# Kernel optimization log

Measured on AMD Instinct MI355X. Metric: run time of the kernel, lower is better.

Reference implementation:

```python
import jax, jax.numpy as jnp
import numpy as np

N = 262144   # number of units (batched instances of the module)
G = 128      # universe_field side length
D = 128      # dimension
RADIUS = 3   # min(3, G//2) == 3

# First D=128 neighborhood offsets in the original triple-loop order (i-major, j, k)
_grid = np.stack(np.meshgrid(np.arange(-RADIUS, RADIUS + 1),
                             np.arange(-RADIUS, RADIUS + 1),
                             np.arange(-RADIUS, RADIUS + 1), indexing='ij'), -1).reshape(-1, 3)[:D]
OI = jnp.asarray(_grid[:, 0], dtype=jnp.int32)
OJ = jnp.asarray(_grid[:, 1], dtype=jnp.int32)
OK = jnp.asarray(_grid[:, 2], dtype=jnp.int32)


def setup_inputs() -> dict:
    key = jax.random.key(0)
    ks = jax.random.split(key, 8)
    return {
        'universe_field': jax.random.normal(ks[0], (G, G, G), jnp.float32),
        'positions': jax.random.uniform(ks[1], (N, 3), jnp.float32) * G,
        'signatures': jax.random.normal(ks[2], (N, D), jnp.float32),
        'offsets': jax.random.normal(ks[3], (N, 3), jnp.float32) * 0.1,
        'W1': jax.random.normal(ks[4], (2 * D, D), jnp.float32) * (1.0 / np.sqrt(2 * D)),
        'b1': jax.random.normal(ks[5], (D,), jnp.float32) * 0.01,
        'W2': jax.random.normal(ks[6], (D, D), jnp.float32) * (1.0 / np.sqrt(D)),
        'b2': jax.random.normal(ks[7], (D,), jnp.float32) * 0.01,
    }


def _sample_local(field, pos):
    # pos: [N,3] float; truncate to int (torch .long()) then clamp, like the original
    pc = jnp.clip(jax.lax.stop_gradient(pos).astype(jnp.int32), 0, G - 1)  # [N,3]
    xx = jnp.clip(pc[:, 0:1] + OI[None, :], 0, G - 1)  # [N,D]
    yy = jnp.clip(pc[:, 1:2] + OJ[None, :], 0, G - 1)
    zz = jnp.clip(pc[:, 2:3] + OK[None, :], 0, G - 1)
    return field[xx, yy, zz]  # [N,D] gathered local field (343 points truncated to D)


def _stability(field, pos, signatures, W1, b1, W2, b2):
    local = _sample_local(field, pos)                       # [N,D]
    combined = jnp.concatenate([signatures, local], axis=-1)  # [N,2D]
    h = jnp.tanh(combined @ W1 + b1)                        # [N,D]
    resp = h @ W2 + b2                                      # [N,D]
    return jnp.linalg.norm(resp - signatures, axis=-1)      # [N]


def reference(universe_field, positions, signatures, offsets, W1, b1, W2, b2):
    stab_old = _stability(universe_field, positions, signatures, W1, b1, W2, b2)
    test_pos = positions + offsets
    stab_new = _stability(universe_field, test_pos, signatures, W1, b1, W2, b2)
    accept = stab_new <= stab_old                           # revert move if new_stab > old_stab
    final_pos = jnp.where(accept[:, None], test_pos, positions)
    stability = jnp.where(accept, stab_new, stab_old)
    return stability, final_pos
```

## Files before the change

### kernel.cpp

```cpp
#include <hip/hip_runtime.h>
#include <hip/hip_bf16.h>

#define NU 262144
#define GG 128
#define PG 134
#define DD 128

typedef __attribute__((ext_vector_type(8))) short short8;
typedef __attribute__((ext_vector_type(4))) float f32x4;

union Frag { short8 s; unsigned u[4]; };

__device__ __forceinline__ unsigned short f2b(float f) {
  union { float f; unsigned u; } v; v.f = f;
  unsigned r = v.u + 0x7fffu + ((v.u >> 16) & 1u);
  return (unsigned short)(r >> 16);
}
__device__ __forceinline__ unsigned cvtpk(float lo, float hi) {
  unsigned r;
  asm("v_cvt_pk_bf16_f32 %0, %1, %2" : "=v"(r) : "v"(lo), "v"(hi));
  return r;
}
__device__ __forceinline__ float unplo(unsigned w) {
  union { unsigned u; float f; } v; v.u = w << 16; return v.f;
}
__device__ __forceinline__ float unphi(unsigned w) {
  union { unsigned u; float f; } v; v.u = w & 0xffff0000u; return v.f;
}

__device__ __forceinline__ float fast_tanh(float x) {
  float e = __expf(fabsf(x) * 2.0f);
  float r = __frcp_rn(e + 1.0f);
  return copysignf(fmaf(-2.0f, r, 1.0f), x);
}

struct alignas(16) RowdT { int v[20]; };
static constexpr RowdT mkrowd() {
  RowdT t{};
  for (int r = 0; r < 20; ++r) {
    int rr = (r < 18) ? r : 18;
    int di = (rr < 18) ? (-3 + rr / 7) : -1;
    int dj = (rr < 18) ? (-3 + rr % 7) : 1;
    t.v[r] = (di * PG + dj) * PG - 3;
  }
  return t;
}
__device__ constexpr RowdT ROWD = mkrowd();

__global__ void prep_field(const float* __restrict__ f, unsigned short* __restrict__ fp) {
  int idx = blockIdx.x * 256 + threadIdx.x;
  if (idx >= PG * PG * PG) return;
  int z = idx % PG, t = idx / PG;
  int y = t % PG, x = t / PG;
  int xx = min(max(x - 3, 0), GG - 1);
  int yy = min(max(y - 3, 0), GG - 1);
  int zz = min(max(z - 3, 0), GG - 1);
  fp[idx] = f2b(f[(xx * GG + yy) * GG + zz]);
}

__global__ void prep_w(const float* __restrict__ W1, const float* __restrict__ W2,
                       unsigned short* __restrict__ wall) {
  int idx = blockIdx.x * 256 + threadIdx.x;
  if (idx >= 6656) return;
  int kt = idx >> 9, nt = (idx >> 6) & 7, ln = idx & 63;
  int n = nt * 16 + (ln & 15), lg = ln >> 4;
  short8 s;
  if (kt < 4) {
    int k0 = kt * 32 + lg * 8;
#pragma unroll
    for (int j = 0; j < 8; ++j) s[j] = (short)f2b(W1[(k0 + j) * DD + n]);
  } else if (kt < 9) {
    int r = (kt - 4) * 4 + lg;
#pragma unroll
    for (int j = 0; j < 8; ++j) {
      bool valid = (r < 18 && j < 7) || (r == 18 && j < 2);
      int row = 128 + ((r < 18) ? (r * 7 + j) : (126 + j));
      s[j] = valid ? (short)f2b(W1[row * DD + n]) : (short)0;
    }
  } else {
    int k0 = (kt - 9) * 32 + lg * 8;
#pragma unroll
    for (int j = 0; j < 8; ++j) s[j] = (short)f2b(W2[(k0 + j) * DD + n]);
  }
  ((short8*)wall)[idx] = s;
}

__global__ __launch_bounds__(512, 4) void atu_main(
    const float* __restrict__ pos, const float* __restrict__ sig,
    const float* __restrict__ offs,
    const float* __restrict__ b1, const float* __restrict__ b2,
    const unsigned short* __restrict__ fpad, const unsigned short* __restrict__ wall,
    float* __restrict__ out_stab, float* __restrict__ out_pos)
{
  __shared__ unsigned short ldsw[2][8192];
  __shared__ unsigned short lds12[4096];
  __shared__ alignas(16) unsigned short ns[8][2048];
  const int tid  = threadIdx.x;
  const int lane = tid & 63;
  const int lg   = lane >> 4, lm = lane & 15;
  const int wid  = tid >> 6;
  int bid = blockIdx.x;
  int swz = (bid & 7) * 256 + (bid >> 3);
  const int ub = swz * 128 + wid * 16;
  const int un = ub + lm;
  char* nsb = (char*)&ns[wid][0];
  const char* wallb = (const char*)wall;
  const char* fpadb = (const char*)fpad;

  int abase[2];
  {
    float px = pos[un * 3 + 0], py = pos[un * 3 + 1], pz = pos[un * 3 + 2];
    float qx = px + offs[un * 3 + 0], qy = py + offs[un * 3 + 1], qz = pz + offs[un * 3 + 2];
    int ax = min(max((int)px, 0), GG - 1), ay = min(max((int)py, 0), GG - 1), az = min(max((int)pz, 0), GG - 1);
    int bx = min(max((int)qx, 0), GG - 1), by = min(max((int)qy, 0), GG - 1), bz = min(max((int)qz, 0), GG - 1);
    abase[0] = ((ax + 3) * PG + (ay + 3)) * PG + (az + 3);
    abase[1] = ((bx + 3) * PG + (by + 3)) * PG + (bz + 3);
  }

#define GLL2(KTA, H)                                                              \
  __builtin_amdgcn_global_load_lds(                                               \
      (const unsigned*)(wallb + (((KTA) * 512 + tid) * 16)),                      \
      (unsigned*)((char*)&ldsw[H][0] + wid * 1024), 16, 0, 0);                    \
  __builtin_amdgcn_global_load_lds(                                               \
      (const unsigned*)(wallb + ((((KTA) + 1) * 512 + tid) * 16)),                \
      (unsigned*)((char*)&ldsw[H][0] + 8192 + wid * 1024), 16, 0, 0);

  GLL2(0, 0)
  __builtin_amdgcn_global_load_lds(
      (const unsigned*)(wallb + ((12 * 512 + tid) * 16)),
      (unsigned*)((char*)lds12 + wid * 1024), 16, 0, 0);
  f32x4 spa = *(const f32x4*)(sig + (size_t)un * DD + lg * 8);
  f32x4 spb = *(const f32x4*)(sig + (size_t)un * DD + lg * 8 + 4);
  short8 rw[5][2];
#pragma unroll
  for (int k = 0; k < 5; ++k) {
    int rd = ROWD.v[k * 4 + lg];
    rw[k][0] = *(const short8*)(fpadb + 2 * (size_t)(abase[0] + rd));
    rw[k][1] = *(const short8*)(fpadb + 2 * (size_t)(abase[1] + rd));
  }

  f32x4 acc[8][2];
#pragma unroll
  for (int nt = 0; nt < 8; ++nt) acc[nt][0] = *(const f32x4*)(b1 + nt * 16 + lg * 4);
  f32x4 acc2[8][2];
  unsigned Q[2][8][2];

  __syncthreads();

#define SIG_KT(KT, HALF)                                                          \
  {                                                                               \
    f32x4 na, nb;                                                                 \
    if ((KT) < 3) {                                                               \
      na = *(const f32x4*)(sig + (size_t)un * DD + ((KT) + 1) * 32 + lg * 8);     \
      nb = *(const f32x4*)(sig + (size_t)un * DD + ((KT) + 1) * 32 + lg * 8 + 4); \
    }                                                                             \
    Frag B;                                                                       \
    B.u[0] = cvtpk(spa[0], spa[1]); B.u[1] = cvtpk(spa[2], spa[3]);               \
    B.u[2] = cvtpk(spb[0], spb[1]); B.u[3] = cvtpk(spb[2], spb[3]);               \
    *(short8*)(nsb + ((KT) * 4 + lg) * 256 + lm * 16) = B.s;                      \
    const char* buf = (const char*)&ldsw[HALF][0] + (((KT) & 1) ? 8192 : 0);      \
    _Pragma("unroll")                                                             \
    for (int nt = 0; nt < 8; ++nt) {                                              \
      short8 af = *(const short8*)(buf + (nt * 64 + lane) * 16);                  \
      acc[nt][0] = __builtin_amdgcn_mfma_f32_16x16x32_bf16(af, B.s, acc[nt][0], 0, 0, 0); \
    }                                                                             \
    if ((KT) < 3) { spa = na; spb = nb; }                                         \
  }

#define ROW_KT(KT, HALF)                                                          \
  {                                                                               \
    const char* buf = (const char*)&ldsw[HALF][0] + (((KT) & 1) ? 8192 : 0);      \
    _Pragma("unroll")                                                             \
    for (int nt = 0; nt < 8; ++nt) {                                              \
      short8 af = *(const short8*)(buf + (nt * 64 + lane) * 16);                  \
      acc[nt][0] = __builtin_amdgcn_mfma_f32_16x16x32_bf16(af, rw[(KT) - 4][0], acc[nt][0], 0, 0, 0); \
      acc[nt][1] = __builtin_amdgcn_mfma_f32_16x16x32_bf16(af, rw[(KT) - 4][1], acc[nt][1], 0, 0, 0); \
    }                                                                             \
  }

#define G2_KT(KT, BUF)                                                            \
  {                                                                               \
    constexpr int kb = (KT) - 9;                                                  \
    Frag W[2];                                                                    \
    _Pragma("unroll")                                                             \
    for (int ut = 0; ut < 2; ++ut) {                                              \
      int qa0 = (int)Q[ut][2 * kb][0],     qa1 = (int)Q[ut][2 * kb][1];           \
      int qb0 = (int)Q[ut][2 * kb + 1][0], qb1 = (int)Q[ut][2 * kb + 1][1];       \
      int r00 = __builtin_amdgcn_ds_bpermute(ad0, qa0);                           \
      int r01 = __builtin_amdgcn_ds_bpermute(ad0, qa1);                           \
      int r10 = __builtin_amdgcn_ds_bpermute(ad1, qa0);                           \
      int r11 = __builtin_amdgcn_ds_bpermute(ad1, qa1);                           \
      int s00 = __builtin_amdgcn_ds_bpermute(ad0, qb0);                           \
      int s01 = __builtin_amdgcn_ds_bpermute(ad0, qb1);                           \
      int s10 = __builtin_amdgcn_ds_bpermute(ad1, qb0);                           \
      int s11 = __builtin_amdgcn_ds_bpermute(ad1, qb1);                           \
      W[ut].u[0] = (unsigned)(hi ? s00 : r00);                                    \
      W[ut].u[1] = (unsigned)(hi ? s01 : r01);                                    \
      W[ut].u[2] = (unsigned)(hi ? s10 : r10);                                    \
      W[ut].u[3] = (unsigned)(hi ? s11 : r11);                                    \
    }                                                                             \
    const char* buf = (BUF);                                                      \
    _Pragma("unroll")                                                             \
    for (int nt = 0; nt < 8; ++nt) {                                              \
      short8 af = *(const short8*)(buf + (nt * 64 + lane) * 16);                  \
      acc2[nt][0] = __builtin_amdgcn_mfma_f32_16x16x32_bf16(af, W[0].s, acc2[nt][0], 0, 0, 0); \
      acc2[nt][1] = __builtin_amdgcn_mfma_f32_16x16x32_bf16(af, W[1].s, acc2[nt][1], 0, 0, 0); \
    }                                                                             \
  }

  const int ad0 = ((((2 * lg) & 3) * 16) + lm) * 4;
  const int ad1 = ((((2 * lg + 1) & 3) * 16) + lm) * 4;
  const bool hi = (lg >= 2);

  GLL2(2, 1)
  SIG_KT(0, 0) SIG_KT(1, 0)
  __syncthreads();

  GLL2(4, 0)
  SIG_KT(2, 1) SIG_KT(3, 1)
  __syncthreads();

#pragma unroll
  for (int nt = 0; nt < 8; ++nt) acc[nt][1] = acc[nt][0];

  GLL2(6, 1)
  ROW_KT(4, 0) ROW_KT(5, 0)
  __syncthreads();

  GLL2(8, 0)
  ROW_KT(6, 1) ROW_KT(7, 1)
  __syncthreads();

  GLL2(10, 1)
  ROW_KT(8, 0)

#pragma unroll
  for (int nt = 0; nt < 8; ++nt) {
#pragma unroll
    for (int ut = 0; ut < 2; ++ut) {
      float h0 = fast_tanh(acc[nt][ut][0]);
      float h1 = fast_tanh(acc[nt][ut][1]);
      float h2 = fast_tanh(acc[nt][ut][2]);
      float h3 = fast_tanh(acc[nt][ut][3]);
      Q[ut][nt][0] = cvtpk(h0, h1);
      Q[ut][nt][1] = cvtpk(h2, h3);
    }
  }
#pragma unroll
  for (int nt = 0; nt < 8; ++nt) {
    f32x4 b2v = *(const f32x4*)(b2 + nt * 16 + lg * 4);
    acc2[nt][0] = b2v; acc2[nt][1] = b2v;
  }

  G2_KT(9, (const char*)&ldsw[0][0] + 8192)
  __syncthreads();

  G2_KT(10, (const char*)&ldsw[1][0])
  G2_KT(11, (const char*)&ldsw[1][0] + 8192)
  G2_KT(12, (const char*)lds12)

  float ssq[2] = {0.f, 0.f};
#pragma unroll
  for (int nt = 0; nt < 8; ++nt) {
    unsigned long long w64 = *(const unsigned long long*)
        (nsb + (nt * 2 + (lg >> 1)) * 256 + lm * 16 + (lg & 1) * 8);
    unsigned w0 = (unsigned)w64, w1 = (unsigned)(w64 >> 32);
    float sv0 = unplo(w0), sv1 = unphi(w0);
    float sv2 = unplo(w1), sv3 = unphi(w1);
#pragma unroll
    for (int ut = 0; ut < 2; ++ut) {
      float d0 = acc2[nt][ut][0] - sv0;
      float d1 = acc2[nt][ut][1] - sv1;
      float d2 = acc2[nt][ut][2] - sv2;
      float d3 = acc2[nt][ut][3] - sv3;
      ssq[ut] = fmaf(d0, d0, ssq[ut]);
      ssq[ut] = fmaf(d1, d1, ssq[ut]);
      ssq[ut] = fmaf(d2, d2, ssq[ut]);
      ssq[ut] = fmaf(d3, d3, ssq[ut]);
    }
  }
  ssq[0] += __shfl_xor(ssq[0], 16, 64); ssq[0] += __shfl_xor(ssq[0], 32, 64);
  ssq[1] += __shfl_xor(ssq[1], 16, 64); ssq[1] += __shfl_xor(ssq[1], 32, 64);

  if (lane < 16) {
    float px = pos[un * 3 + 0], py = pos[un * 3 + 1], pz = pos[un * 3 + 2];
    float ox = offs[un * 3 + 0], oy = offs[un * 3 + 1], oz = offs[un * 3 + 2];
    bool ok = ssq[1] <= ssq[0];
    out_stab[un] = sqrtf(ok ? ssq[1] : ssq[0]);
    out_pos[un * 3 + 0] = ok ? px + ox : px;
    out_pos[un * 3 + 1] = ok ? py + oy : py;
    out_pos[un * 3 + 2] = ok ? pz + oz : pz;
  }
#undef GLL2
#undef SIG_KT
#undef ROW_KT
#undef G2_KT
}

extern "C" void kernel_launch(void* const* d_in, const int* in_sizes, int n_in,
                              void* d_out, int out_size, void* d_ws, size_t ws_size,
                              hipStream_t stream) {
  const float* field = (const float*)d_in[0];
  const float* pos   = (const float*)d_in[1];
  const float* sig   = (const float*)d_in[2];
  const float* offs  = (const float*)d_in[3];
  const float* W1    = (const float*)d_in[4];
  const float* b1    = (const float*)d_in[5];
  const float* W2    = (const float*)d_in[6];
  const float* b2    = (const float*)d_in[7];
  float* out_stab = (float*)d_out;
  float* out_pos  = out_stab + NU;

  char* ws = (char*)d_ws;
  unsigned short* fpad = (unsigned short*)ws;
  unsigned short* wall = (unsigned short*)(ws + 4812800);

  prep_field<<<(PG * PG * PG + 255) / 256, 256, 0, stream>>>(field, fpad);
  prep_w<<<26, 256, 0, stream>>>(W1, W2, wall);
  atu_main<<<NU / 128, 512, 0, stream>>>(pos, sig, offs, b1, b2,
                                         fpad, wall, out_stab, out_pos);
}
```

Measured before the change: 134.2 us.

## Bin units by spatial cell to improve locality of field gathers

Adds a counting-sort pipeline (histogram, scan, scatter) that groups units by 8x8x8 grid cell, then runs the main kernel over the permuted order so neighbouring units gather overlapping field regions. Signatures are read indirectly through the permutation and outputs are scattered back. It adds three small kernels, atomics and extra traffic for permuted positions and offsets, and makes signature reads non-coalesced across rows. The sorted path is only used when the workspace is large enough.

```diff
diff --git a/kernel.cpp b/kernel.cpp
--- a/kernel.cpp
+++ b/kernel.cpp
@@ -5,6 +5,7 @@
 #define GG 128
 #define PG 134
 #define DD 128
+#define NCELL 4096
 
 typedef __attribute__((ext_vector_type(8))) short short8;
 typedef __attribute__((ext_vector_type(4))) float f32x4;
@@ -46,6 +47,13 @@
   return t;
 }
 __device__ constexpr RowdT ROWD = mkrowd();
+
+__device__ __forceinline__ int cell_of(float px, float py, float pz) {
+  int cx = min(max((int)px, 0), GG - 1) >> 3;
+  int cy = min(max((int)py, 0), GG - 1) >> 3;
+  int cz = min(max((int)pz, 0), GG - 1) >> 3;
+  return (cx << 8) | (cy << 4) | cz;
+}
 
 __global__ void prep_field(const float* __restrict__ f, unsigned short* __restrict__ fp) {
   int idx = blockIdx.x * 256 + threadIdx.x;
@@ -59,8 +67,9 @@
 }
 
 __global__ void prep_w(const float* __restrict__ W1, const float* __restrict__ W2,
-                       unsigned short* __restrict__ wall) {
+                       unsigned short* __restrict__ wall, int* __restrict__ cursor) {
   int idx = blockIdx.x * 256 + threadIdx.x;
+  if (cursor && idx < NCELL) cursor[idx] = 0;
   if (idx >= 6656) return;
   int kt = idx >> 9, nt = (idx >> 6) & 7, ln = idx & 63;
   int n = nt * 16 + (ln & 15), lg = ln >> 4;
@@ -85,9 +94,46 @@
   ((short8*)wall)[idx] = s;
 }
 
+__global__ void hist_k(const float* __restrict__ pos, int* __restrict__ cursor) {
+  int u = blockIdx.x * 256 + threadIdx.x;
+  atomicAdd(&cursor[cell_of(pos[u * 3], pos[u * 3 + 1], pos[u * 3 + 2])], 1);
+}
+__global__ void scan_k(int* __restrict__ cursor) {
+  __shared__ int sums[256];
+  int t = threadIdx.x;
+  int local[16];
+  int partial = 0;
+#pragma unroll
+  for (int j = 0; j < 16; ++j) { local[j] = cursor[t * 16 + j]; partial += local[j]; }
+  sums[t] = partial;
+  __syncthreads();
+  for (int off = 1; off < 256; off <<= 1) {
+    int v = (t >= off) ? sums[t - off] : 0;
+    __syncthreads();
+    sums[t] += v;
+    __syncthreads();
+  }
+  int excl = sums[t] - partial;
+#pragma unroll
+  for (int j = 0; j < 16; ++j) { cursor[t * 16 + j] = excl; excl += local[j]; }
+}
+__global__ void scatter_k(const float* __restrict__ pos, const float* __restrict__ offs,
+                          int* __restrict__ cursor, int* __restrict__ perm,
+                          float* __restrict__ posP, float* __restrict__ offsP) {
+  int u = blockIdx.x * 256 + threadIdx.x;
+  float px = pos[u * 3 + 0], py = pos[u * 3 + 1], pz = pos[u * 3 + 2];
+  int dst = atomicAdd(&cursor[cell_of(px, py, pz)], 1);
+  perm[dst] = u;
+  posP[dst * 3 + 0] = px; posP[dst * 3 + 1] = py; posP[dst * 3 + 2] = pz;
+  offsP[dst * 3 + 0] = offs[u * 3 + 0];
+  offsP[dst * 3 + 1] = offs[u * 3 + 1];
+  offsP[dst * 3 + 2] = offs[u * 3 + 2];
+}
+
+template<bool SORT>
 __global__ __launch_bounds__(512, 4) void atu_main(
     const float* __restrict__ pos, const float* __restrict__ sig,
-    const float* __restrict__ offs,
+    const float* __restrict__ offs, const int* __restrict__ perm,
     const float* __restrict__ b1, const float* __restrict__ b2,
     const unsigned short* __restrict__ fpad, const unsigned short* __restrict__ wall,
     float* __restrict__ out_stab, float* __restrict__ out_pos)
@@ -103,6 +149,7 @@
   int swz = (bid & 7) * 256 + (bid >> 3);
   const int ub = swz * 128 + wid * 16;
   const int un = ub + lm;
+  const int pv = SORT ? perm[un] : un;
   char* nsb = (char*)&ns[wid][0];
   const char* wallb = (const char*)wall;
   const char* fpadb = (const char*)fpad;
@@ -129,8 +176,8 @@
   __builtin_amdgcn_global_load_lds(
       (const unsigned*)(wallb + ((12 * 512 + tid) * 16)),
       (unsigned*)((char*)lds12 + wid * 1024), 16, 0, 0);
-  f32x4 spa = *(const f32x4*)(sig + (size_t)un * DD + lg * 8);
-  f32x4 spb = *(const f32x4*)(sig + (size_t)un * DD + lg * 8 + 4);
+  f32x4 spa = *(const f32x4*)(sig + (size_t)pv * DD + lg * 8);
+  f32x4 spb = *(const f32x4*)(sig + (size_t)pv * DD + lg * 8 + 4);
   short8 rw[5][2];
 #pragma unroll
   for (int k = 0; k < 5; ++k) {
@@ -151,8 +198,8 @@
   {                                                                               \
     f32x4 na, nb;                                                                 \
     if ((KT) < 3) {                                                               \
-      na = *(const f32x4*)(sig + (size_t)un * DD + ((KT) + 1) * 32 + lg * 8);     \
-      nb = *(const f32x4*)(sig + (size_t)un * DD + ((KT) + 1) * 32 + lg * 8 + 4); \
+      na = *(const f32x4*)(sig + (size_t)pv * DD + ((KT) + 1) * 32 + lg * 8);     \
+      nb = *(const f32x4*)(sig + (size_t)pv * DD + ((KT) + 1) * 32 + lg * 8 + 4); \
     }                                                                             \
     Frag B;                                                                       \
     B.u[0] = cvtpk(spa[0], spa[1]); B.u[1] = cvtpk(spa[2], spa[3]);               \
@@ -286,10 +333,10 @@
     float px = pos[un * 3 + 0], py = pos[un * 3 + 1], pz = pos[un * 3 + 2];
     float ox = offs[un * 3 + 0], oy = offs[un * 3 + 1], oz = offs[un * 3 + 2];
     bool ok = ssq[1] <= ssq[0];
-    out_stab[un] = sqrtf(ok ? ssq[1] : ssq[0]);
-    out_pos[un * 3 + 0] = ok ? px + ox : px;
-    out_pos[un * 3 + 1] = ok ? py + oy : py;
-    out_pos[un * 3 + 2] = ok ? pz + oz : pz;
+    out_stab[pv] = sqrtf(ok ? ssq[1] : ssq[0]);
+    out_pos[pv * 3 + 0] = ok ? px + ox : px;
+    out_pos[pv * 3 + 1] = ok ? py + oy : py;
+    out_pos[pv * 3 + 2] = ok ? pz + oz : pz;
   }
 #undef GLL2
 #undef SIG_KT
@@ -312,11 +359,26 @@
   float* out_pos  = out_stab + NU;
 
   char* ws = (char*)d_ws;
-  unsigned short* fpad = (unsigned short*)ws;
-  unsigned short* wall = (unsigned short*)(ws + 4812800);
+  unsigned short* fpad  = (unsigned short*)ws;
+  unsigned short* wall  = (unsigned short*)(ws + 4812800);
+  float*          posP  = (float*)(ws + 4919296);
+  float*          offsP = (float*)(ws + 8065024);
+  int*            perm  = (int*)(ws + 11210752);
+  int*            cursor= (int*)(ws + 12259328);
+  const size_t need_sort = 12275712ull;
 
   prep_field<<<(PG * PG * PG + 255) / 256, 256, 0, stream>>>(field, fpad);
-  prep_w<<<26, 256, 0, stream>>>(W1, W2, wall);
-  atu_main<<<NU / 128, 512, 0, stream>>>(pos, sig, offs, b1, b2,
-                                         fpad, wall, out_stab, out_pos);
-}
+
+  if (ws_size >= need_sort) {
+    prep_w<<<26, 256, 0, stream>>>(W1, W2, wall, cursor);
+    hist_k<<<NU / 256, 256, 0, stream>>>(pos, cursor);
+    scan_k<<<1, 256, 0, stream>>>(cursor);
+    scatter_k<<<NU / 256, 256, 0, stream>>>(pos, offs, cursor, perm, posP, offsP);
+    atu_main<true><<<NU / 128, 512, 0, stream>>>(posP, sig, offsP, perm, b1, b2,
+                                                 fpad, wall, out_stab, out_pos);
+  } else {
+    prep_w<<<26, 256, 0, stream>>>(W1, W2, wall, nullptr);
+    atu_main<false><<<NU / 128, 512, 0, stream>>>(pos, sig, offs, nullptr, b1, b2,
+                                                  fpad, wall, out_stab, out_pos);
+  }
+}
```

After: 177.1 us. 32.0% more time.
